# Kernel tuning notes

Hardware: AMD Instinct MI355X
Metric: run time of the kernel (lower is better)

Reference implementation:

```python
import jax, jax.numpy as jnp
import numpy as np

N, C, F = 16384, 2048, 512


def setup_inputs() -> dict:
    key = jax.random.key(0)
    kx, km = jax.random.split(key)
    x = jax.random.normal(kx, (N, F), dtype=jnp.float32)
    means = jax.random.normal(km, (C, F), dtype=jnp.float32)
    return {"x": x, "means": means}


def reference(x, means):
    # Negative Euclidean distance scores: -sqrt(sum_f (x[n,f] - means[c,f])^2)
    # intermediate the naive expand/pow/sum formulation materializes).
    x_sq = jnp.sum(x * x, axis=-1, keepdims=True)          # [N, 1]
    m_sq = jnp.sum(means * means, axis=-1)                 # [C]
    cross = jnp.einsum('nf,cf->nc', x, means)              # [N, C]
    d2 = jnp.maximum(x_sq + m_sq[None, :] - 2.0 * cross, 0.0)
    return -jnp.sqrt(d2)
```

## Files before the change

### kernel.cpp

```cpp
#include <hip/hip_runtime.h>
#include <hip/hip_bf16.h>

constexpr int N_ROWS = 16384;
constexpr int C_CLS  = 2048;
constexpr int F_DIM  = 512;

typedef __bf16 bf16x8 __attribute__((ext_vector_type(8)));
typedef float  f32x16 __attribute__((ext_vector_type(16)));

__global__ __launch_bounds__(256) void prep_rows(
    const float* __restrict__ x,
    const float* __restrict__ means,
    __hip_bfloat162* __restrict__ xb,
    __hip_bfloat162* __restrict__ mb,
    float* __restrict__ xsq,
    float* __restrict__ msq)
{
    int row = blockIdx.x;
    const float* src;
    __hip_bfloat162* dst;
    float* sq;
    if (row < N_ROWS) { src = x; dst = xb; sq = xsq; }
    else { row -= N_ROWS; src = means; dst = mb; sq = msq; }

    const int tid = threadIdx.x;
    const float2 v = ((const float2*)(src + (size_t)row * F_DIM))[tid];

    __hip_bfloat162 p;
    p.x = __float2bfloat16(v.x);
    p.y = __float2bfloat16(v.y);
    dst[(size_t)row * (F_DIM / 2) + tid] = p;

    float ss = v.x * v.x + v.y * v.y;
    #pragma unroll
    for (int off = 32; off > 0; off >>= 1) ss += __shfl_down(ss, off);

    __shared__ float red[4];
    if ((tid & 63) == 0) red[tid >> 6] = ss;
    __syncthreads();
    if (tid == 0) sq[row] = red[0] + red[1] + red[2] + red[3];
}

__device__ __forceinline__ void async_copy16(const __hip_bfloat16* g,
                                             __hip_bfloat16* l)
{
    __builtin_amdgcn_global_load_lds(
        (const __attribute__((address_space(1))) unsigned int*)g,
        (__attribute__((address_space(3))) unsigned int*)l,
        16, 0, 0);
}

__global__ __launch_bounds__(256) void ncm_gemm(
    const __hip_bfloat16* __restrict__ xb,
    const __hip_bfloat16* __restrict__ mb,
    const float* __restrict__ xsq,
    const float* __restrict__ msq,
    float* __restrict__ out)
{
    constexpr int BK = 32, NKT = F_DIM / BK;

    __shared__ alignas(16) __hip_bfloat16 sA[2][128 * BK];
    __shared__ alignas(16) __hip_bfloat16 sB[2][128 * BK];

    const int tid  = threadIdx.x;
    const int wave = tid >> 6;
    const int lane = tid & 63;
    const int wm   = wave >> 1;
    const int wn   = wave & 1;

    const int band  = blockIdx.x & 127;
    const int ctile = blockIdx.x >> 7;
    const int row0 = band * 128;
    const int col0 = ctile * 128;

    const int srow   = lane >> 2;
    const int schunk = (lane & 3) ^ ((lane >> 3) & 3);
    const __hip_bfloat16* gA =
        xb + (size_t)(row0 + wave * 32 + srow) * F_DIM + schunk * 8;
    const __hip_bfloat16* gB =
        mb + (size_t)(col0 + wave * 32 + srow) * F_DIM + schunk * 8;

    f32x16 acc[2][2] = {};

    const int lrow  = lane & 31;
    const int khalf = lane >> 5;
    const int rsw   = (lrow >> 1) & 3;

    #pragma unroll
    for (int i = 0; i < 2; ++i) {
        async_copy16(gA + (size_t)i * 16 * F_DIM,
                     &sA[0][(wave * 32 + i * 16) * BK]);
        async_copy16(gB + (size_t)i * 16 * F_DIM,
                     &sB[0][(wave * 32 + i * 16) * BK]);
    }

    for (int kt = 0; kt < NKT; ++kt) {
        const int p = kt & 1;
        __syncthreads();

        if (kt + 1 < NKT) {
            const int k0n = (kt + 1) * BK;
            #pragma unroll
            for (int i = 0; i < 2; ++i) {
                async_copy16(gA + (size_t)i * 16 * F_DIM + k0n,
                             &sA[1 - p][(wave * 32 + i * 16) * BK]);
                async_copy16(gB + (size_t)i * 16 * F_DIM + k0n,
                             &sB[1 - p][(wave * 32 + i * 16) * BK]);
            }
        }

        #pragma unroll
        for (int s = 0; s < 2; ++s) {
            const int pos = ((2 * s + khalf) ^ rsw) * 8;
            bf16x8 af[2], bfr[2];
            #pragma unroll
            for (int mt = 0; mt < 2; ++mt)
                af[mt] = *(const bf16x8*)
                    &sA[p][(wm * 64 + mt * 32 + lrow) * BK + pos];
            #pragma unroll
            for (int nt = 0; nt < 2; ++nt)
                bfr[nt] = *(const bf16x8*)
                    &sB[p][(wn * 64 + nt * 32 + lrow) * BK + pos];
            #pragma unroll
            for (int mt = 0; mt < 2; ++mt)
                #pragma unroll
                for (int nt = 0; nt < 2; ++nt)
                    acc[mt][nt] = __builtin_amdgcn_mfma_f32_32x32x16_bf16(
                        af[mt], bfr[nt], acc[mt][nt], 0, 0, 0);
        }
    }

    #pragma unroll
    for (int mt = 0; mt < 2; ++mt) {
        const int rbase = row0 + wm * 64 + mt * 32 + 4 * khalf;
        float xs[16];
        #pragma unroll
        for (int r = 0; r < 16; ++r)
            xs[r] = xsq[rbase + (r & 3) + 8 * (r >> 2)];
        #pragma unroll
        for (int nt = 0; nt < 2; ++nt) {
            const int col = col0 + wn * 64 + nt * 32 + lrow;
            const float ms = msq[col];
            #pragma unroll
            for (int r = 0; r < 16; ++r) {
                const int row = rbase + (r & 3) + 8 * (r >> 2);
                const float d2 =
                    fmaxf(xs[r] + ms - 2.0f * acc[mt][nt][r], 0.0f);
                out[(size_t)row * C_CLS + col] = -sqrtf(d2);
            }
        }
    }
}

extern "C" void kernel_launch(void* const* d_in, const int* in_sizes, int n_in,
                              void* d_out, int out_size, void* d_ws,
                              size_t ws_size, hipStream_t stream)
{
    const float* x     = (const float*)d_in[0];
    const float* means = (const float*)d_in[1];
    float* out = (float*)d_out;

    char* ws = (char*)d_ws;
    __hip_bfloat16* xb = (__hip_bfloat16*)ws;
    __hip_bfloat16* mb = (__hip_bfloat16*)(ws + (size_t)N_ROWS * F_DIM * 2);
    float* xsq = (float*)(ws + (size_t)(N_ROWS + C_CLS) * F_DIM * 2);
    float* msq = xsq + N_ROWS;

    prep_rows<<<N_ROWS + C_CLS, 256, 0, stream>>>(
        x, means, (__hip_bfloat162*)xb, (__hip_bfloat162*)mb, xsq, msq);

    ncm_gemm<<<dim3(2048), 256, 0, stream>>>(xb, mb, xsq, msq, out);
}
```

Measured before the change: 198.9 us.

## Enlarge GEMM tiles to 256x256 with 3-stage pipeline and one-wave-per-row prep

The GEMM moves from 128x128 tiles with 4 waves to 256x256 tiles with 8 waves, each wave holding 4x2 MFMA accumulators. The shared-memory ring goes from two stages to three, and each iteration waits with an explicit vmcnt wait plus a barrier instead of __syncthreads. A swizzled block index groups neighbouring blocks for better L2 reuse. The prep kernel now gives each row to a single wave using float4 loads and 16-byte bf16 stores, which drops the shared-memory reduction. This cuts global load traffic per FLOP and synchronisation overhead, at the cost of more registers and 96KB of dynamic LDS, which may limit occupancy.

```diff
diff --git a/kernel.cpp b/kernel.cpp
--- a/kernel.cpp
+++ b/kernel.cpp
@@ -8,37 +8,41 @@
 typedef __bf16 bf16x8 __attribute__((ext_vector_type(8)));
 typedef float  f32x16 __attribute__((ext_vector_type(16)));
 
+struct alignas(16) B8 { __hip_bfloat162 h[4]; };
+
 __global__ __launch_bounds__(256) void prep_rows(
     const float* __restrict__ x,
     const float* __restrict__ means,
-    __hip_bfloat162* __restrict__ xb,
-    __hip_bfloat162* __restrict__ mb,
+    B8* __restrict__ xb,
+    B8* __restrict__ mb,
     float* __restrict__ xsq,
     float* __restrict__ msq)
 {
-    int row = blockIdx.x;
-    const float* src;
-    __hip_bfloat162* dst;
-    float* sq;
+    const int tid  = threadIdx.x;
+    const int wv   = tid >> 6;
+    const int lane = tid & 63;
+    int row = blockIdx.x * 4 + wv;
+
+    const float* src; B8* dst; float* sq;
     if (row < N_ROWS) { src = x; dst = xb; sq = xsq; }
     else { row -= N_ROWS; src = means; dst = mb; sq = msq; }
 
-    const int tid = threadIdx.x;
-    const float2 v = ((const float2*)(src + (size_t)row * F_DIM))[tid];
-
-    __hip_bfloat162 p;
-    p.x = __float2bfloat16(v.x);
-    p.y = __float2bfloat16(v.y);
-    dst[(size_t)row * (F_DIM / 2) + tid] = p;
-
-    float ss = v.x * v.x + v.y * v.y;
+    const float4* s4 = (const float4*)(src + (size_t)row * F_DIM);
+    const float4 a = s4[lane * 2 + 0];
+    const float4 b = s4[lane * 2 + 1];
+
+    B8 pk;
+    pk.h[0].x = __float2bfloat16(a.x); pk.h[0].y = __float2bfloat16(a.y);
+    pk.h[1].x = __float2bfloat16(a.z); pk.h[1].y = __float2bfloat16(a.w);
+    pk.h[2].x = __float2bfloat16(b.x); pk.h[2].y = __float2bfloat16(b.y);
+    pk.h[3].x = __float2bfloat16(b.z); pk.h[3].y = __float2bfloat16(b.w);
+    dst[(size_t)row * (F_DIM / 8) + lane] = pk;
+
+    float ss = a.x * a.x + a.y * a.y + a.z * a.z + a.w * a.w
+             + b.x * b.x + b.y * b.y + b.z * b.z + b.w * b.w;
     #pragma unroll
     for (int off = 32; off > 0; off >>= 1) ss += __shfl_down(ss, off);
-
-    __shared__ float red[4];
-    if ((tid & 63) == 0) red[tid >> 6] = ss;
-    __syncthreads();
-    if (tid == 0) sq[row] = red[0] + red[1] + red[2] + red[3];
+    if (lane == 0) sq[row] = ss;
 }
 
 __device__ __forceinline__ void async_copy16(const __hip_bfloat16* g,
@@ -50,28 +54,32 @@
         16, 0, 0);
 }
 
-__global__ __launch_bounds__(256) void ncm_gemm(
+constexpr int BM = 256, BN = 256, BK = 32;
+constexpr int NKT     = F_DIM / BK;
+constexpr int STAGE_E = (BM + BN) * BK;
+constexpr int NSTAGE  = 3;
+constexpr size_t SMEM_BYTES = (size_t)NSTAGE * STAGE_E * sizeof(__hip_bfloat16);
+
+__global__ __launch_bounds__(512, 2) void ncm_gemm(
     const __hip_bfloat16* __restrict__ xb,
     const __hip_bfloat16* __restrict__ mb,
     const float* __restrict__ xsq,
     const float* __restrict__ msq,
     float* __restrict__ out)
 {
-    constexpr int BK = 32, NKT = F_DIM / BK;
-
-    __shared__ alignas(16) __hip_bfloat16 sA[2][128 * BK];
-    __shared__ alignas(16) __hip_bfloat16 sB[2][128 * BK];
+    extern __shared__ __hip_bfloat16 smem[];
 
     const int tid  = threadIdx.x;
     const int wave = tid >> 6;
     const int lane = tid & 63;
-    const int wm   = wave >> 1;
-    const int wn   = wave & 1;
-
-    const int band  = blockIdx.x & 127;
-    const int ctile = blockIdx.x >> 7;
-    const int row0 = band * 128;
-    const int col0 = ctile * 128;
+    const int wm   = wave >> 2;
+    const int wn   = wave & 3;
+
+    const int wgid  = (blockIdx.x & 7) * 64 + (blockIdx.x >> 3);
+    const int ctile = wgid & 7;
+    const int band  = wgid >> 3;
+    const int row0 = band * BM;
+    const int col0 = ctile * BN;
 
     const int srow   = lane >> 2;
     const int schunk = (lane & 3) ^ ((lane >> 3) & 3);
@@ -80,59 +88,70 @@
     const __hip_bfloat16* gB =
         mb + (size_t)(col0 + wave * 32 + srow) * F_DIM + schunk * 8;
 
-    f32x16 acc[2][2] = {};
+    f32x16 acc[4][2] = {};
 
     const int lrow  = lane & 31;
     const int khalf = lane >> 5;
     const int rsw   = (lrow >> 1) & 3;
-
-    #pragma unroll
-    for (int i = 0; i < 2; ++i) {
-        async_copy16(gA + (size_t)i * 16 * F_DIM,
-                     &sA[0][(wave * 32 + i * 16) * BK]);
-        async_copy16(gB + (size_t)i * 16 * F_DIM,
-                     &sB[0][(wave * 32 + i * 16) * BK]);
-    }
-
+    const int pos0  = ((0 + khalf) ^ rsw) * 8;
+    const int pos1  = ((2 + khalf) ^ rsw) * 8;
+
+    int aoff[4], boff[2];
+    #pragma unroll
+    for (int mt = 0; mt < 4; ++mt)
+        aoff[mt] = (wm * 128 + mt * 32 + lrow) * BK;
+    #pragma unroll
+    for (int nt = 0; nt < 2; ++nt)
+        boff[nt] = BM * BK + (wn * 64 + nt * 32 + lrow) * BK;
+
+    auto stage = [&](int s, int kt) {
+        __hip_bfloat16* ba = smem + s * STAGE_E + (wave * 32) * BK;
+        __hip_bfloat16* bb = ba + BM * BK;
+        const size_t k0 = (size_t)kt * BK;
+        #pragma unroll
+        for (int i = 0; i < 2; ++i) {
+            async_copy16(gA + (size_t)(i * 16) * F_DIM + k0, ba + i * 16 * BK);
+            async_copy16(gB + (size_t)(i * 16) * F_DIM + k0, bb + i * 16 * BK);
+        }
+    };
+
+    stage(0, 0);
+    stage(1, 1);
+
+    int p = 0, pn = 2;
     for (int kt = 0; kt < NKT; ++kt) {
-        const int p = kt & 1;
-        __syncthreads();
-
-        if (kt + 1 < NKT) {
-            const int k0n = (kt + 1) * BK;
-            #pragma unroll
-            for (int i = 0; i < 2; ++i) {
-                async_copy16(gA + (size_t)i * 16 * F_DIM + k0n,
-                             &sA[1 - p][(wave * 32 + i * 16) * BK]);
-                async_copy16(gB + (size_t)i * 16 * F_DIM + k0n,
-                             &sB[1 - p][(wave * 32 + i * 16) * BK]);
-            }
-        }
-
+        if (kt < NKT - 1) asm volatile("s_waitcnt vmcnt(4)" ::: "memory");
+        else              asm volatile("s_waitcnt vmcnt(0)" ::: "memory");
+        __builtin_amdgcn_s_barrier();
+        asm volatile("" ::: "memory");
+
+        if (kt + 2 < NKT) stage(pn, kt + 2);
+
+        const __hip_bfloat16* sA = smem + p * STAGE_E;
         #pragma unroll
         for (int s = 0; s < 2; ++s) {
-            const int pos = ((2 * s + khalf) ^ rsw) * 8;
-            bf16x8 af[2], bfr[2];
-            #pragma unroll
-            for (int mt = 0; mt < 2; ++mt)
-                af[mt] = *(const bf16x8*)
-                    &sA[p][(wm * 64 + mt * 32 + lrow) * BK + pos];
+            const int pos = s ? pos1 : pos0;
+            bf16x8 af[4], bfr[2];
+            #pragma unroll
+            for (int mt = 0; mt < 4; ++mt)
+                af[mt] = *(const bf16x8*)&sA[aoff[mt] + pos];
             #pragma unroll
             for (int nt = 0; nt < 2; ++nt)
-                bfr[nt] = *(const bf16x8*)
-                    &sB[p][(wn * 64 + nt * 32 + lrow) * BK + pos];
-            #pragma unroll
-            for (int mt = 0; mt < 2; ++mt)
+                bfr[nt] = *(const bf16x8*)&sA[boff[nt] + pos];
+            #pragma unroll
+            for (int mt = 0; mt < 4; ++mt)
                 #pragma unroll
                 for (int nt = 0; nt < 2; ++nt)
                     acc[mt][nt] = __builtin_amdgcn_mfma_f32_32x32x16_bf16(
                         af[mt], bfr[nt], acc[mt][nt], 0, 0, 0);
         }
+        p  = (p  == 2) ? 0 : p  + 1;
+        pn = (pn == 2) ? 0 : pn + 1;
     }
 
     #pragma unroll
-    for (int mt = 0; mt < 2; ++mt) {
-        const int rbase = row0 + wm * 64 + mt * 32 + 4 * khalf;
+    for (int mt = 0; mt < 4; ++mt) {
+        const int rbase = row0 + wm * 128 + mt * 32 + 4 * khalf;
         float xs[16];
         #pragma unroll
         for (int r = 0; r < 16; ++r)
@@ -166,8 +185,17 @@
     float* xsq = (float*)(ws + (size_t)(N_ROWS + C_CLS) * F_DIM * 2);
     float* msq = xsq + N_ROWS;
 
-    prep_rows<<<N_ROWS + C_CLS, 256, 0, stream>>>(
-        x, means, (__hip_bfloat162*)xb, (__hip_bfloat162*)mb, xsq, msq);
-
-    ncm_gemm<<<dim3(2048), 256, 0, stream>>>(xb, mb, xsq, msq, out);
-}
+    static bool attr_done = false;
+    if (!attr_done) {
+        hipFuncSetAttribute((const void*)ncm_gemm,
+                            hipFuncAttributeMaxDynamicSharedMemorySize,
+                            (int)SMEM_BYTES);
+        attr_done = true;
+    }
+
+    prep_rows<<<(N_ROWS + C_CLS) / 4, 256, 0, stream>>>(
+        x, means, (B8*)xb, (B8*)mb, xsq, msq);
+
+    ncm_gemm<<<dim3(512), dim3(512), SMEM_BYTES, stream>>>(
+        xb, mb, xsq, msq, out);
+}
```

Result: faster. 191.8 us (-3.6%).
